# Kernel tuning notes

Measured on AMD Instinct MI355X. Metric: run time of the kernel, lower is better.

## Reference

```python
import jax, jax.numpy as jnp
import numpy as np

N_NODES = 100000
N_EDGES = 3200000
D = 256
REPEAT = 2
FACTOR = 0.5


def setup_inputs() -> dict:
    key = jax.random.key(0)
    k1, k2, k3, k4, k5, k6 = jax.random.split(key, 6)
    x = jax.random.normal(k1, (N_NODES, D), dtype=jnp.float32)
    vals = jax.random.uniform(k2, (N_EDGES,), dtype=jnp.float32)
    # Xavier-ish scale for linear weights
    W0 = jax.random.normal(k3, (D, D), dtype=jnp.float32) / np.sqrt(D)
    W1 = jax.random.normal(k4, (D, D), dtype=jnp.float32) / np.sqrt(D)
    rows = jax.random.randint(k5, (N_EDGES,), 0, N_NODES, dtype=jnp.int32)
    cols = jax.random.randint(k6, (N_EDGES,), 0, N_NODES, dtype=jnp.int32)
    return {"x": x, "vals": vals, "W0": W0, "W1": W1, "rows": rows, "cols": cols}


def reference(x, vals, W0, W1, rows, cols):
    # support is sparse [N, N] in COO: support[rows[e], cols[e]] = vals[e]
    def spmm(h):
        # gather source-node features, scale by edge weight, scatter-add to dst
        return jax.ops.segment_sum(vals[:, None] * h[cols], rows,
                                   num_segments=N_NODES)

    h = x
    for W, act in ((W0, jax.nn.relu), (W1, lambda v: v)):
        # _propagate: repeated SpMM with scalar factor
        for _ in range(REPEAT):
            h = spmm(h) * FACTOR
        # linear (no bias) + activation
        h = act(h @ W)
    return h
```

## Files before the change

kernel.cpp:

```cpp
#include <hip/hip_runtime.h>
#include <hip/hip_bf16.h>
#include <hip/hip_fp16.h>

#define N_D 256
#define NBLK 832

typedef __attribute__((ext_vector_type(8))) short bf16x8;
typedef __attribute__((ext_vector_type(4))) float f32x4;

__device__ __forceinline__ unsigned short f2bf(float f) {
  union { float f; unsigned u; } c; c.f = f;
  unsigned u = c.u;
  return (unsigned short)((u + 0x7fffu + ((u >> 16) & 1u)) >> 16);
}
__device__ __forceinline__ float asf(unsigned u) {
  union { unsigned u; float f; } c; c.u = u;
  return c.f;
}
__device__ __forceinline__ int grp_of(int r, unsigned gmagic) {
  int g = (int)(((unsigned long long)(unsigned)r * gmagic) >> 37);
  return min(g, 7);
}

template <bool AF32>
__device__ __forceinline__ void gemm_core(
    const void* __restrict__ H, const unsigned short* __restrict__ WT,
    unsigned short* __restrict__ C, int M, int bid) {
  const int wave = threadIdx.x >> 6;
  const int lane = threadIdx.x & 63;
  const int m = lane & 15;
  const int p = lane >> 4;
  const int row0 = bid * 128 + wave * 32;

  f32x4 acc0[16], acc1[16];
#pragma unroll
  for (int i = 0; i < 16; ++i) {
    acc0[i] = (f32x4){0.f, 0.f, 0.f, 0.f};
    acc1[i] = (f32x4){0.f, 0.f, 0.f, 0.f};
  }

  const int r0 = row0 + m;
  const int r1 = row0 + 16 + m;
  const bool ok0 = r0 < M, ok1 = r1 < M;

  for (int k0 = 0; k0 < N_D; k0 += 32) {
    bf16x8 a0 = {0,0,0,0,0,0,0,0}, a1 = {0,0,0,0,0,0,0,0};
    if (AF32) {
      if (ok0) {
        const float* ap = (const float*)H + (size_t)r0 * N_D + k0 + p * 8;
        const float4 f0 = *reinterpret_cast<const float4*>(ap);
        const float4 f1 = *reinterpret_cast<const float4*>(ap + 4);
        a0[0]=f2bf(f0.x); a0[1]=f2bf(f0.y); a0[2]=f2bf(f0.z); a0[3]=f2bf(f0.w);
        a0[4]=f2bf(f1.x); a0[5]=f2bf(f1.y); a0[6]=f2bf(f1.z); a0[7]=f2bf(f1.w);
      }
      if (ok1) {
        const float* ap = (const float*)H + (size_t)r1 * N_D + k0 + p * 8;
        const float4 f0 = *reinterpret_cast<const float4*>(ap);
        const float4 f1 = *reinterpret_cast<const float4*>(ap + 4);
        a1[0]=f2bf(f0.x); a1[1]=f2bf(f0.y); a1[2]=f2bf(f0.z); a1[3]=f2bf(f0.w);
        a1[4]=f2bf(f1.x); a1[5]=f2bf(f1.y); a1[6]=f2bf(f1.z); a1[7]=f2bf(f1.w);
      }
    } else {
      if (ok0) a0 = *reinterpret_cast<const bf16x8*>(
          (const unsigned short*)H + (size_t)r0 * N_D + k0 + p * 8);
      if (ok1) a1 = *reinterpret_cast<const bf16x8*>(
          (const unsigned short*)H + (size_t)r1 * N_D + k0 + p * 8);
    }
#pragma unroll
    for (int nt = 0; nt < 16; ++nt) {
      const bf16x8 b = *reinterpret_cast<const bf16x8*>(
          WT + (size_t)(nt * 16 + m) * N_D + k0 + p * 8);
      acc0[nt] = __builtin_amdgcn_mfma_f32_16x16x32_bf16(a0, b, acc0[nt], 0, 0, 0);
      acc1[nt] = __builtin_amdgcn_mfma_f32_16x16x32_bf16(a1, b, acc1[nt], 0, 0, 0);
    }
  }

#pragma unroll
  for (int nt = 0; nt < 16; ++nt) {
    const int col = nt * 16 + m;
#pragma unroll
    for (int rr = 0; rr < 4; ++rr) {
      const int ra = row0 + p * 4 + rr;
      const int rb = ra + 16;
      if (ra < M) C[(size_t)ra * N_D + col] = f2bf(acc0[nt][rr]);
      if (rb < M) C[(size_t)rb * N_D + col] = f2bf(acc1[nt][rr]);
    }
  }
}

__global__ __launch_bounds__(256) void wconv_kernel(
    const float* __restrict__ W0, const float* __restrict__ W1,
    unsigned short* __restrict__ WT0, unsigned short* __restrict__ WT1) {
  const int w = blockIdx.x >> 8;
  const int k = blockIdx.x & 255;
  const int n = threadIdx.x;
  const float* W = w ? W1 : W0;
  unsigned short* WT = w ? WT1 : WT0;
  WT[(size_t)n * N_D + k] = f2bf(W[(size_t)k * N_D + n]);
}

__global__ __launch_bounds__(256) void fat1_kernel(
    const int* __restrict__ rows, int* __restrict__ cnt8, int* __restrict__ cntT,
    int n_edges, unsigned gmagic, int M,
    const float* __restrict__ x, const unsigned short* __restrict__ WT0,
    unsigned short* __restrict__ hB) {
  if (blockIdx.x >= NBLK) {
    gemm_core<true>(x, WT0, hB, M, blockIdx.x - NBLK);
    return;
  }
  __shared__ int lcnt[8];
  if (threadIdx.x < 8) lcnt[threadIdx.x] = 0;
  __syncthreads();
  int* __restrict__ cnt = cnt8 + (size_t)(blockIdx.x & 7) * M;
  for (int e = blockIdx.x * 256 + threadIdx.x; e < n_edges; e += NBLK * 256) {
    const int r = rows[e];
    atomicAdd(&cnt[r], 1);
    atomicAdd(&lcnt[grp_of(r, gmagic)], 1);
  }
  __syncthreads();
  if (threadIdx.x < 8) cntT[threadIdx.x * NBLK + blockIdx.x] = lcnt[threadIdx.x];
}

__global__ __launch_bounds__(256) void sumcnt_kernel(
    const int* __restrict__ cnt8, int* __restrict__ cnts,
    int* __restrict__ bsum, int M) {
  __shared__ int wred[4];
  const int i = blockIdx.x * 256 + threadIdx.x;
  int s = 0;
  if (i < M) {
#pragma unroll
    for (int k = 0; k < 8; ++k) s += cnt8[(size_t)k * M + i];
    cnts[i] = s;
  }
  int t = s;
#pragma unroll
  for (int off = 32; off; off >>= 1) t += __shfl_down(t, off, 64);
  if ((threadIdx.x & 63) == 0) wred[threadIdx.x >> 6] = t;
  __syncthreads();
  if (threadIdx.x == 0) bsum[blockIdx.x] = wred[0] + wred[1] + wred[2] + wred[3];
}

__device__ void scan256(const int* __restrict__ in, int* __restrict__ out, int n) {
  __shared__ int swsum[4];
  __shared__ int carry_sh;
  const int tid = threadIdx.x;
  const int lane = tid & 63;
  const int wid = tid >> 6;
  if (tid == 0) carry_sh = 0;
  __syncthreads();
  for (int base = 0; base < n; base += 1024) {
    const int i0 = base + tid * 4;
    int4 v = make_int4(0, 0, 0, 0);
    if (i0 + 3 < n) v = *reinterpret_cast<const int4*>(in + i0);
    else {
      if (i0     < n) v.x = in[i0];
      if (i0 + 1 < n) v.y = in[i0 + 1];
      if (i0 + 2 < n) v.z = in[i0 + 2];
    }
    const int s1 = v.x, s2 = s1 + v.y, s3 = s2 + v.z, s4 = s3 + v.w;
    int ws = s4;
#pragma unroll
    for (int off = 1; off < 64; off <<= 1) {
      int o = __shfl_up(ws, off, 64);
      if (lane >= off) ws += o;
    }
    if (lane == 63) swsum[wid] = ws;
    __syncthreads();
    if (wid == 0) {
      int t = (lane < 4) ? swsum[lane] : 0;
#pragma unroll
      for (int off = 1; off < 4; off <<= 1) {
        int o = __shfl_up(t, off, 64);
        if (lane >= off) t += o;
      }
      if (lane < 4) swsum[lane] = t;
    }
    __syncthreads();
    const int carry = carry_sh;
    const int tbase = carry + (wid ? swsum[wid - 1] : 0) + ws - s4;
    if (i0     < n) out[i0]     = tbase;
    if (i0 + 1 < n) out[i0 + 1] = tbase + s1;
    if (i0 + 2 < n) out[i0 + 2] = tbase + s2;
    if (i0 + 3 < n) out[i0 + 3] = tbase + s3;
    __syncthreads();
    if (tid == 0) carry_sh = carry + swsum[3];
    __syncthreads();
  }
  if (tid == 0) out[n] = carry_sh;
}

__global__ __launch_bounds__(256) void scan2_kernel(
    const int* __restrict__ bsum, int* __restrict__ bofs, int Mb,
    const int* __restrict__ cntT, int* __restrict__ pofsT) {
  if (blockIdx.x == 0) scan256(bsum, bofs, Mb);
  else                 scan256(cntT, pofsT, 8 * NBLK);
}

__global__ __launch_bounds__(256) void build2_kernel(
    const int* __restrict__ cnts, const int* __restrict__ bofs,
    int* __restrict__ row_ptr, int* __restrict__ cursor, int M, int Mb,
    const int* __restrict__ rows, const int* __restrict__ cols,
    const float* __restrict__ vals, const int* __restrict__ pofsT,
    int2* __restrict__ part, int n_edges, unsigned gmagic) {
  __shared__ int shmem[8];
  if (blockIdx.x < Mb) {
    const int tid = threadIdx.x;
    const int lane = tid & 63;
    const int wid = tid >> 6;
    const int i = blockIdx.x * 256 + tid;
    const int v = (i < M) ? cnts[i] : 0;
    int s = v;
#pragma unroll
    for (int off = 1; off < 64; off <<= 1) {
      int o = __shfl_up(s, off, 64);
      if (lane >= off) s += o;
    }
    if (lane == 63) shmem[wid] = s;
    __syncthreads();
    int add = 0;
    for (int k = 0; k < wid; ++k) add += shmem[k];
    const int excl = bofs[blockIdx.x] + add + s - v;
    if (i < M) { row_ptr[i] = excl; cursor[i] = excl; }
    if (i == M) row_ptr[M] = bofs[Mb];
  } else {
    const int pb = blockIdx.x - Mb;
    if (threadIdx.x < 8) shmem[threadIdx.x] = pofsT[threadIdx.x * NBLK + pb];
    __syncthreads();
    for (int e = pb * 256 + threadIdx.x; e < n_edges; e += NBLK * 256) {
      const int r = rows[e];
      const int g = grp_of(r, gmagic);
      const int slot = atomicAdd(&shmem[g], 1);
      const unsigned short hb = __half_as_ushort(__float2half_rn(vals[e] * 0.5f));
      int2 rv;
      rv.x = r;
      rv.y = (int)(((unsigned)cols[e] << 15) | ((unsigned)hb >> 1));
      part[slot] = rv;
    }
  }
}

__global__ __launch_bounds__(256) void scatter2_kernel(
    const int2* __restrict__ part, const int* __restrict__ pofsT,
    int* __restrict__ cursor, unsigned* __restrict__ colpack) {
  const int g  = blockIdx.x & 7;
  const int bk = blockIdx.x >> 3;
  const int nb = gridDim.x >> 3;
  const int s0 = pofsT[g * NBLK];
  const int s1 = pofsT[(g + 1) * NBLK];
  for (int i = s0 + bk * 256 + threadIdx.x; i < s1; i += nb * 256) {
    const int2 rv = part[i];
    const int pos = atomicAdd(&cursor[rv.x], 1);
    colpack[pos] = (unsigned)rv.y;
  }
}

template <bool RELU, bool F32OUT>
__global__ __launch_bounds__(256) void spmm_slice(
    const unsigned short* __restrict__ hin, const int* __restrict__ row_ptr,
    const unsigned* __restrict__ colpack, void* __restrict__ hout,
    int n_nodes) {
  const int slice = blockIdx.x & 3;
  const int lane = threadIdx.x & 63;
  const int half = lane >> 5;
  const int sub  = lane & 31;
  const int wgid = ((blockIdx.x >> 2) * 256 + threadIdx.x) >> 6;
  const int node = wgid * 2 + half;
  const bool ok = node < n_nodes;
  int start = 0, end = 0;
  if (ok) { start = row_ptr[node]; end = row_ptr[node + 1]; }

  const unsigned* __restrict__ hinw = reinterpret_cast<const unsigned*>(hin);
  const int fofs = slice * 32 + sub;
  const int sbase = half << 5;

  float acc0 = 0.f, acc1 = 0.f;

  for (int base = start; base < end; base += 32) {
    const int cnt = min(32, end - base);
    unsigned u = 0;
    if (base + sub < end) u = __builtin_nontemporal_load(&colpack[base + sub]);
    for (int t = 0; t < cnt; t += 8) {
      unsigned hv[8];
      float v[8];
#pragma unroll
      for (int j = 0; j < 8; ++j) {
        const unsigned ue = (unsigned)__shfl((int)u, sbase + t + j, 64);
        const int c = (int)(ue >> 15);
        v[j] = __half2float(__ushort_as_half((unsigned short)(ue << 1)));
        hv[j] = hinw[(size_t)c * 128 + fofs];
      }
#pragma unroll
      for (int j = 0; j < 8; ++j) {
        acc0 += v[j] * asf(hv[j] << 16);
        acc1 += v[j] * asf(hv[j] & 0xffff0000u);
      }
    }
  }
  if (ok) {
    if (RELU) { acc0 = fmaxf(acc0, 0.f); acc1 = fmaxf(acc1, 0.f); }
    if (F32OUT) {
      reinterpret_cast<float2*>(hout)[(size_t)node * 128 + fofs] =
          make_float2(acc0, acc1);
    } else {
      reinterpret_cast<unsigned*>(hout)[(size_t)node * 128 + fofs] =
          (unsigned)f2bf(acc0) | ((unsigned)f2bf(acc1) << 16);
    }
  }
}

__global__ __launch_bounds__(256) void gemm3_bf16(
    const unsigned short* __restrict__ H, const unsigned short* __restrict__ WT,
    unsigned short* __restrict__ C, int M) {
  gemm_core<false>(H, WT, C, M, blockIdx.x);
}

extern "C" void kernel_launch(void* const* d_in, const int* in_sizes, int n_in,
                              void* d_out, int out_size, void* d_ws, size_t ws_size,
                              hipStream_t stream) {
  const float* x    = (const float*)d_in[0];
  const float* vals = (const float*)d_in[1];
  const float* W0   = (const float*)d_in[2];
  const float* W1   = (const float*)d_in[3];
  const int*   rows = (const int*)d_in[4];
  const int*   cols = (const int*)d_in[5];

  const int n_edges = in_sizes[1];
  const int M = in_sizes[0] / N_D;
  const size_t n_feat = (size_t)M * N_D;

  char* ws = (char*)d_ws;
  unsigned short* hA      = (unsigned short*)(ws);
  unsigned*       colpack = (unsigned*)(ws + 51200000);
  int*            row_ptr = (int*)(ws + 64000000);
  int*            cursor  = (int*)(ws + 64400128);
  int*            cnt8    = (int*)(ws + 64800256);
  int*            cnts    = (int*)(ws + 68000384);
  int*            bsum    = (int*)(ws + 68400512);
  int*            bofs    = (int*)(ws + 68402560);
  int*            cntT    = (int*)(ws + 68406656);
  int*            pofsT   = (int*)(ws + 68433536);
  unsigned short* wt0     = (unsigned short*)(ws + 68487296);
  unsigned short* wt1     = (unsigned short*)(ws + 68618368);
  unsigned short* hB   = (unsigned short*)d_out;
  unsigned short* hC   = (unsigned short*)d_out + n_feat;
  int2*           part = (int2*)((char*)d_out + 51200000);

  const int Mb = (M + 255) / 256;
  const int sblocks = 4 * ((M + 7) / 8);
  const int gblocks = (M + 127) / 128;
  const int rpg = (M + 7) / 8;
  const unsigned gmagic = (unsigned)(((1ULL << 37) + rpg - 1) / (unsigned long long)rpg);

  hipMemsetAsync(cnt8, 0, (size_t)8 * M * sizeof(int), stream);
  wconv_kernel<<<512, 256, 0, stream>>>(W0, W1, wt0, wt1);
  fat1_kernel<<<NBLK + gblocks, 256, 0, stream>>>(rows, cnt8, cntT, n_edges,
                                                  gmagic, M, x, wt0, hB);
  sumcnt_kernel<<<Mb, 256, 0, stream>>>(cnt8, cnts, bsum, M);
  scan2_kernel<<<2, 256, 0, stream>>>(bsum, bofs, Mb, cntT, pofsT);
  build2_kernel<<<Mb + NBLK, 256, 0, stream>>>(cnts, bofs, row_ptr, cursor, M, Mb,
                                               rows, cols, vals, pofsT, part,
                                               n_edges, gmagic);
  scatter2_kernel<<<NBLK, 256, 0, stream>>>(part, pofsT, cursor, colpack);

  spmm_slice<false, false><<<sblocks, 256, 0, stream>>>(hB, row_ptr, colpack, hA, M);
  spmm_slice<true,  false><<<sblocks, 256, 0, stream>>>(hA, row_ptr, colpack, hB, M);

  gemm3_bf16<<<gblocks, 256, 0, stream>>>(hB, wt1, hC, M);
  spmm_slice<false, false><<<sblocks, 256, 0, stream>>>(hC, row_ptr, colpack, hA, M);
  spmm_slice<false, true ><<<sblocks, 256, 0, stream>>>(hA, row_ptr, colpack, d_out, M);
}
```

Baseline: 1.220 ms.

## Build CSR via LDS-local per-group histograms instead of global atomics

New measurement: 1.125 ms. -7.8%, faster.

```diff
diff --git a/kernel.cpp b/kernel.cpp
--- a/kernel.cpp
+++ b/kernel.cpp
@@ -4,6 +4,8 @@
 
 #define N_D 256
 #define NBLK 832
+#define CPB 104
+#define RPG_MAX 12512
 
 typedef __attribute__((ext_vector_type(8))) short bf16x8;
 typedef __attribute__((ext_vector_type(4))) float f32x4;
@@ -88,59 +90,44 @@
   }
 }
 
-__global__ __launch_bounds__(256) void wconv_kernel(
+__global__ __launch_bounds__(256) void gemm3_f32(
+    const float* __restrict__ H, const unsigned short* __restrict__ WT,
+    unsigned short* __restrict__ C, int M) {
+  gemm_core<true>(H, WT, C, M, blockIdx.x);
+}
+__global__ __launch_bounds__(256) void gemm3_bf16(
+    const unsigned short* __restrict__ H, const unsigned short* __restrict__ WT,
+    unsigned short* __restrict__ C, int M) {
+  gemm_core<false>(H, WT, C, M, blockIdx.x);
+}
+
+__global__ __launch_bounds__(256) void p0_kernel(
+    const int* __restrict__ rows, int* __restrict__ cntT,
+    int n_edges, unsigned gmagic,
     const float* __restrict__ W0, const float* __restrict__ W1,
     unsigned short* __restrict__ WT0, unsigned short* __restrict__ WT1) {
-  const int w = blockIdx.x >> 8;
-  const int k = blockIdx.x & 255;
-  const int n = threadIdx.x;
-  const float* W = w ? W1 : W0;
-  unsigned short* WT = w ? WT1 : WT0;
-  WT[(size_t)n * N_D + k] = f2bf(W[(size_t)k * N_D + n]);
-}
-
-__global__ __launch_bounds__(256) void fat1_kernel(
-    const int* __restrict__ rows, int* __restrict__ cnt8, int* __restrict__ cntT,
-    int n_edges, unsigned gmagic, int M,
-    const float* __restrict__ x, const unsigned short* __restrict__ WT0,
-    unsigned short* __restrict__ hB) {
   if (blockIdx.x >= NBLK) {
-    gemm_core<true>(x, WT0, hB, M, blockIdx.x - NBLK);
+    const int b = blockIdx.x - NBLK;
+    const int w = b >> 8;
+    const int k = b & 255;
+    const int n = threadIdx.x;
+    const float* W = w ? W1 : W0;
+    unsigned short* WT = w ? WT1 : WT0;
+    WT[(size_t)n * N_D + k] = f2bf(W[(size_t)k * N_D + n]);
     return;
   }
-  __shared__ int lcnt[8];
-  if (threadIdx.x < 8) lcnt[threadIdx.x] = 0;
-  __syncthreads();
-  int* __restrict__ cnt = cnt8 + (size_t)(blockIdx.x & 7) * M;
+  __shared__ int l8[8];
+  if (threadIdx.x < 8) l8[threadIdx.x] = 0;
+  __syncthreads();
   for (int e = blockIdx.x * 256 + threadIdx.x; e < n_edges; e += NBLK * 256) {
-    const int r = rows[e];
-    atomicAdd(&cnt[r], 1);
-    atomicAdd(&lcnt[grp_of(r, gmagic)], 1);
-  }
-  __syncthreads();
-  if (threadIdx.x < 8) cntT[threadIdx.x * NBLK + blockIdx.x] = lcnt[threadIdx.x];
-}
-
-__global__ __launch_bounds__(256) void sumcnt_kernel(
-    const int* __restrict__ cnt8, int* __restrict__ cnts,
-    int* __restrict__ bsum, int M) {
-  __shared__ int wred[4];
-  const int i = blockIdx.x * 256 + threadIdx.x;
-  int s = 0;
-  if (i < M) {
-#pragma unroll
-    for (int k = 0; k < 8; ++k) s += cnt8[(size_t)k * M + i];
-    cnts[i] = s;
-  }
-  int t = s;
-#pragma unroll
-  for (int off = 32; off; off >>= 1) t += __shfl_down(t, off, 64);
-  if ((threadIdx.x & 63) == 0) wred[threadIdx.x >> 6] = t;
-  __syncthreads();
-  if (threadIdx.x == 0) bsum[blockIdx.x] = wred[0] + wred[1] + wred[2] + wred[3];
-}
-
-__device__ void scan256(const int* __restrict__ in, int* __restrict__ out, int n) {
+    atomicAdd(&l8[grp_of(rows[e], gmagic)], 1);
+  }
+  __syncthreads();
+  if (threadIdx.x < 8) cntT[threadIdx.x * NBLK + blockIdx.x] = l8[threadIdx.x];
+}
+
+__global__ __launch_bounds__(256) void scan_one(
+    const int* __restrict__ in, int* __restrict__ out, int n) {
   __shared__ int swsum[4];
   __shared__ int carry_sh;
   const int tid = threadIdx.x;
@@ -189,67 +176,113 @@
   if (tid == 0) out[n] = carry_sh;
 }
 
-__global__ __launch_bounds__(256) void scan2_kernel(
-    const int* __restrict__ bsum, int* __restrict__ bofs, int Mb,
-    const int* __restrict__ cntT, int* __restrict__ pofsT) {
-  if (blockIdx.x == 0) scan256(bsum, bofs, Mb);
-  else                 scan256(cntT, pofsT, 8 * NBLK);
-}
-
-__global__ __launch_bounds__(256) void build2_kernel(
-    const int* __restrict__ cnts, const int* __restrict__ bofs,
-    int* __restrict__ row_ptr, int* __restrict__ cursor, int M, int Mb,
+__global__ __launch_bounds__(256) void partition_kernel(
     const int* __restrict__ rows, const int* __restrict__ cols,
     const float* __restrict__ vals, const int* __restrict__ pofsT,
     int2* __restrict__ part, int n_edges, unsigned gmagic) {
-  __shared__ int shmem[8];
-  if (blockIdx.x < Mb) {
-    const int tid = threadIdx.x;
-    const int lane = tid & 63;
-    const int wid = tid >> 6;
-    const int i = blockIdx.x * 256 + tid;
-    const int v = (i < M) ? cnts[i] : 0;
-    int s = v;
-#pragma unroll
-    for (int off = 1; off < 64; off <<= 1) {
-      int o = __shfl_up(s, off, 64);
-      if (lane >= off) s += o;
-    }
-    if (lane == 63) shmem[wid] = s;
-    __syncthreads();
-    int add = 0;
-    for (int k = 0; k < wid; ++k) add += shmem[k];
-    const int excl = bofs[blockIdx.x] + add + s - v;
-    if (i < M) { row_ptr[i] = excl; cursor[i] = excl; }
-    if (i == M) row_ptr[M] = bofs[Mb];
-  } else {
-    const int pb = blockIdx.x - Mb;
-    if (threadIdx.x < 8) shmem[threadIdx.x] = pofsT[threadIdx.x * NBLK + pb];
-    __syncthreads();
-    for (int e = pb * 256 + threadIdx.x; e < n_edges; e += NBLK * 256) {
-      const int r = rows[e];
-      const int g = grp_of(r, gmagic);
-      const int slot = atomicAdd(&shmem[g], 1);
-      const unsigned short hb = __half_as_ushort(__float2half_rn(vals[e] * 0.5f));
-      int2 rv;
-      rv.x = r;
-      rv.y = (int)(((unsigned)cols[e] << 15) | ((unsigned)hb >> 1));
-      part[slot] = rv;
-    }
-  }
-}
-
-__global__ __launch_bounds__(256) void scatter2_kernel(
+  __shared__ int lofs[8];
+  if (threadIdx.x < 8) lofs[threadIdx.x] = pofsT[threadIdx.x * NBLK + blockIdx.x];
+  __syncthreads();
+  for (int e = blockIdx.x * 256 + threadIdx.x; e < n_edges; e += NBLK * 256) {
+    const int r = rows[e];
+    const int g = grp_of(r, gmagic);
+    const int slot = atomicAdd(&lofs[g], 1);
+    const unsigned short hb = __half_as_ushort(__float2half_rn(vals[e] * 0.5f));
+    int2 rv;
+    rv.x = r;
+    rv.y = (int)(((unsigned)cols[e] << 15) | ((unsigned)hb >> 1));
+    part[slot] = rv;
+  }
+}
+
+__global__ __launch_bounds__(256) void hist_kernel(
     const int2* __restrict__ part, const int* __restrict__ pofsT,
-    int* __restrict__ cursor, unsigned* __restrict__ colpack) {
-  const int g  = blockIdx.x & 7;
-  const int bk = blockIdx.x >> 3;
-  const int nb = gridDim.x >> 3;
-  const int s0 = pofsT[g * NBLK];
-  const int s1 = pofsT[(g + 1) * NBLK];
-  for (int i = s0 + bk * 256 + threadIdx.x; i < s1; i += nb * 256) {
+    int* __restrict__ cntc, int M, int rpg) {
+  const int g = blockIdx.x & 7;
+  const int b = blockIdx.x >> 3;
+  const int r0 = g * rpg;
+  const int nr = min(rpg, M - r0);
+  __shared__ int lh[RPG_MAX];
+  for (int r = threadIdx.x; r < nr; r += 256) lh[r] = 0;
+  __syncthreads();
+  const int s0 = pofsT[g * NBLK + b * CPB];
+  const int s1 = pofsT[g * NBLK + (b + 1) * CPB];
+  for (int i = s0 + threadIdx.x; i < s1; i += 256) {
+    atomicAdd(&lh[part[i].x - r0], 1);
+  }
+  __syncthreads();
+  int* dst = cntc + (size_t)(g * 8 + b) * rpg;
+  for (int r = threadIdx.x; r < nr; r += 256) dst[r] = lh[r];
+}
+
+__global__ __launch_bounds__(256) void sumcnt2_kernel(
+    int* __restrict__ cntc, int* __restrict__ cnts,
+    int* __restrict__ bsum, int M, int rpg) {
+  __shared__ int wred[4];
+  const int i = blockIdx.x * 256 + threadIdx.x;
+  int s = 0;
+  if (i < M) {
+    const int g = i / rpg;
+    const int rr = i - g * rpg;
+    int* base = cntc + (size_t)g * 8 * rpg + rr;
+#pragma unroll
+    for (int b = 0; b < 8; ++b) {
+      const int c = base[(size_t)b * rpg];
+      base[(size_t)b * rpg] = s;
+      s += c;
+    }
+    cnts[i] = s;
+  }
+  int t = s;
+#pragma unroll
+  for (int off = 32; off; off >>= 1) t += __shfl_down(t, off, 64);
+  if ((threadIdx.x & 63) == 0) wred[threadIdx.x >> 6] = t;
+  __syncthreads();
+  if (threadIdx.x == 0) bsum[blockIdx.x] = wred[0] + wred[1] + wred[2] + wred[3];
+}
+
+__global__ __launch_bounds__(256) void apply_kernel(
+    const int* __restrict__ cnts, const int* __restrict__ bofs,
+    int* __restrict__ row_ptr, int M) {
+  __shared__ int wsum[4];
+  const int tid = threadIdx.x;
+  const int lane = tid & 63;
+  const int wid = tid >> 6;
+  const int i = blockIdx.x * 256 + tid;
+  const int v = (i < M) ? cnts[i] : 0;
+  int s = v;
+#pragma unroll
+  for (int off = 1; off < 64; off <<= 1) {
+    int o = __shfl_up(s, off, 64);
+    if (lane >= off) s += o;
+  }
+  if (lane == 63) wsum[wid] = s;
+  __syncthreads();
+  int add = 0;
+  for (int k = 0; k < wid; ++k) add += wsum[k];
+  const int excl = bofs[blockIdx.x] + add + s - v;
+  if (i < M) row_ptr[i] = excl;
+  if (i == M) row_ptr[M] = bofs[gridDim.x];
+}
+
+__global__ __launch_bounds__(256) void scatter3_kernel(
+    const int2* __restrict__ part, const int* __restrict__ pofsT,
+    const int* __restrict__ row_ptr, const int* __restrict__ cntc,
+    unsigned* __restrict__ colpack, int M, int rpg) {
+  const int g = blockIdx.x & 7;
+  const int b = blockIdx.x >> 3;
+  const int r0 = g * rpg;
+  const int nr = min(rpg, M - r0);
+  __shared__ int lc[RPG_MAX];
+  const int* pfx = cntc + (size_t)(g * 8 + b) * rpg;
+  for (int r = threadIdx.x; r < nr; r += 256)
+    lc[r] = row_ptr[r0 + r] + pfx[r];
+  __syncthreads();
+  const int s0 = pofsT[g * NBLK + b * CPB];
+  const int s1 = pofsT[g * NBLK + (b + 1) * CPB];
+  for (int i = s0 + threadIdx.x; i < s1; i += 256) {
     const int2 rv = part[i];
-    const int pos = atomicAdd(&cursor[rv.x], 1);
+    const int pos = atomicAdd(&lc[rv.x - r0], 1);
     colpack[pos] = (unsigned)rv.y;
   }
 }
@@ -308,12 +341,6 @@
   }
 }
 
-__global__ __launch_bounds__(256) void gemm3_bf16(
-    const unsigned short* __restrict__ H, const unsigned short* __restrict__ WT,
-    unsigned short* __restrict__ C, int M) {
-  gemm_core<false>(H, WT, C, M, blockIdx.x);
-}
-
 extern "C" void kernel_launch(void* const* d_in, const int* in_sizes, int n_in,
                               void* d_out, int out_size, void* d_ws, size_t ws_size,
                               hipStream_t stream) {
@@ -332,15 +359,14 @@
   unsigned short* hA      = (unsigned short*)(ws);
   unsigned*       colpack = (unsigned*)(ws + 51200000);
   int*            row_ptr = (int*)(ws + 64000000);
-  int*            cursor  = (int*)(ws + 64400128);
-  int*            cnt8    = (int*)(ws + 64800256);
-  int*            cnts    = (int*)(ws + 68000384);
-  int*            bsum    = (int*)(ws + 68400512);
-  int*            bofs    = (int*)(ws + 68402560);
-  int*            cntT    = (int*)(ws + 68406656);
-  int*            pofsT   = (int*)(ws + 68433536);
-  unsigned short* wt0     = (unsigned short*)(ws + 68487296);
-  unsigned short* wt1     = (unsigned short*)(ws + 68618368);
+  int*            cnts    = (int*)(ws + 64400128);
+  int*            cntc    = (int*)(ws + 64800256);
+  int*            bsum    = (int*)(ws + 68000384);
+  int*            bofs    = (int*)(ws + 68002944);
+  int*            cntT    = (int*)(ws + 68005504);
+  int*            pofsT   = (int*)(ws + 68033536);
+  unsigned short* wt0     = (unsigned short*)(ws + 68061568);
+  unsigned short* wt1     = (unsigned short*)(ws + 68192640);
   unsigned short* hB   = (unsigned short*)d_out;
   unsigned short* hC   = (unsigned short*)d_out + n_feat;
   int2*           part = (int2*)((char*)d_out + 51200000);
@@ -351,16 +377,18 @@
   const int rpg = (M + 7) / 8;
   const unsigned gmagic = (unsigned)(((1ULL << 37) + rpg - 1) / (unsigned long long)rpg);
 
-  hipMemsetAsync(cnt8, 0, (size_t)8 * M * sizeof(int), stream);
-  wconv_kernel<<<512, 256, 0, stream>>>(W0, W1, wt0, wt1);
-  fat1_kernel<<<NBLK + gblocks, 256, 0, stream>>>(rows, cnt8, cntT, n_edges,
-                                                  gmagic, M, x, wt0, hB);
-  sumcnt_kernel<<<Mb, 256, 0, stream>>>(cnt8, cnts, bsum, M);
-  scan2_kernel<<<2, 256, 0, stream>>>(bsum, bofs, Mb, cntT, pofsT);
-  build2_kernel<<<Mb + NBLK, 256, 0, stream>>>(cnts, bofs, row_ptr, cursor, M, Mb,
-                                               rows, cols, vals, pofsT, part,
-                                               n_edges, gmagic);
-  scatter2_kernel<<<NBLK, 256, 0, stream>>>(part, pofsT, cursor, colpack);
+  p0_kernel<<<NBLK + 512, 256, 0, stream>>>(rows, cntT, n_edges, gmagic,
+                                            W0, W1, wt0, wt1);
+  scan_one<<<1, 256, 0, stream>>>(cntT, pofsT, 8 * NBLK);
+  gemm3_f32<<<gblocks, 256, 0, stream>>>(x, wt0, hB, M);
+  partition_kernel<<<NBLK, 256, 0, stream>>>(rows, cols, vals, pofsT, part,
+                                             n_edges, gmagic);
+  hist_kernel<<<64, 256, 0, stream>>>(part, pofsT, cntc, M, rpg);
+  sumcnt2_kernel<<<Mb, 256, 0, stream>>>(cntc, cnts, bsum, M, rpg);
+  scan_one<<<1, 256, 0, stream>>>(bsum, bofs, Mb);
+  apply_kernel<<<Mb, 256, 0, stream>>>(cnts, bofs, row_ptr, M);
+  scatter3_kernel<<<64, 256, 0, stream>>>(part, pofsT, row_ptr, cntc,
+                                          colpack, M, rpg);
 
   spmm_slice<false, false><<<sblocks, 256, 0, stream>>>(hB, row_ptr, colpack, hA, M);
   spmm_slice<true,  false><<<sblocks, 256, 0, stream>>>(hA, row_ptr, colpack, hB, M);
```
